# Kernel optimization log

Measured on AMD Instinct MI355X. Metric: run time of the kernel, lower is better.

## Reference

```python
import jax, jax.numpy as jnp
import numpy as np
import math

EPS_RMS = 1.1920929e-07  # torch nn.RMSNorm default eps = finfo(float32).eps
EPS_DEN = 1e-6


def rmsnorm(x, gamma):
    ms = jnp.mean(x * x, axis=-1, keepdims=True)
    return x * jax.lax.rsqrt(ms + EPS_RMS) * gamma


def setup_inputs() -> dict:
    key = jax.random.key(0)
    ks = jax.random.split(key, 8)
    B, T, K, D = 4, 4096, 256, 1024
    x_tokens = jax.random.normal(ks[0], (B, T, D), dtype=jnp.float32)
    ctx = jax.random.normal(ks[1], (B, K, D), dtype=jnp.float32)
    idx = jnp.sort(jax.random.randint(ks[2], (B, T), 0, K), axis=-1)
    s = 1.0 / math.sqrt(D)
    Wq = jax.random.normal(ks[3], (D, D), dtype=jnp.float32) * s
    Wk = jax.random.normal(ks[4], (D, D), dtype=jnp.float32) * s
    Wv = jax.random.normal(ks[5], (D, D), dtype=jnp.float32) * s
    Wo = jax.random.normal(ks[6], (D, D), dtype=jnp.float32) * s
    return {
        'x_tokens': x_tokens, 'ctx': ctx, 'ctx_index_per_token': idx,
        'gamma_q': jnp.ones((D,), jnp.float32), 'gamma_kv': jnp.ones((D,), jnp.float32),
        'Wq': Wq, 'Wk': Wk, 'Wv': Wv, 'Wo': Wo,
    }


def reference(x_tokens, ctx, ctx_index_per_token, gamma_q, gamma_kv, Wq, Wk, Wv, Wo):
    B, T, D = x_tokens.shape
    K = ctx.shape[1]
    H = 16
    hd = D // H

    def split(x):  # (B,S,D) -> (B,H,S,hd)
        return x.reshape(B, -1, H, hd).transpose(0, 2, 1, 3)

    q = split(rmsnorm(x_tokens, gamma_q) @ Wq.T)
    kn = rmsnorm(ctx, gamma_kv)
    k = split(kn @ Wk.T)
    v = split(kn @ Wv.T)

    # band mask: |ctx_pos - idx| <= 1, shape (B,1,T,K)
    ctx_pos = jnp.arange(K)[None, None, :]
    mask = (jnp.abs(ctx_pos - ctx_index_per_token[:, :, None]) <= 1)[:, None]

    scores = jnp.einsum('bhqd,bhkd->bhqk', q, k) / math.sqrt(hd)
    w = jnp.square(jax.nn.relu(scores))
    w = jnp.where(mask, w, 0.0)
    denom = jnp.maximum(w.sum(-1, keepdims=True), EPS_DEN)
    out = jnp.einsum('bhqk,bhkd->bhqd', w / denom, v)
    out = out.transpose(0, 2, 1, 3).reshape(B, T, D)
    return x_tokens + out @ Wo.T
```

## Files before the change

kernel.cpp:

```cpp
#include <hip/hip_runtime.h>
#include <hip/hip_bf16.h>
#include <stdint.h>

#define D_DIM 1024

using f32x4  = __attribute__((ext_vector_type(4))) float;
using short8 = __attribute__((ext_vector_type(8))) short;

__device__ __forceinline__ float bf2f(unsigned short u) {
    union { unsigned int i; float f; } v; v.i = ((unsigned int)u) << 16; return v.f;
}
__device__ __forceinline__ unsigned short f2bf(float f) {
    union { float f; unsigned int i; } v; v.f = f;
    unsigned int x = v.i;
    return (unsigned short)((x + 0x7fffu + ((x >> 16) & 1u)) >> 16);
}
__device__ __forceinline__ void gload16(const void* g, void* l) {
    __builtin_amdgcn_global_load_lds(
        (const __attribute__((address_space(1))) void*)g,
        (__attribute__((address_space(3))) void*)l, 16, 0, 0);
}

__global__ __launch_bounds__(256)
void convw_kernel(const float* __restrict__ Wk, const float* __restrict__ Wv,
                  const float* __restrict__ Wo, const float* __restrict__ gkv,
                  unsigned short* __restrict__ wk_hi, unsigned short* __restrict__ wk_lo,
                  unsigned short* __restrict__ wv_hi, unsigned short* __restrict__ wv_lo,
                  unsigned short* __restrict__ wo_b)
{
    const int e   = (blockIdx.x * 256 + threadIdx.x) * 4;
    const int sel = e >> 20;
    const int off = e & 0xFFFFF;
    const float* src = sel == 0 ? Wk : sel == 1 ? Wv : Wo;
    float4 v = *(const float4*)(src + off);
    if (sel < 2) {
        float4 g = *(const float4*)(gkv + (off & 1023));
        v.x *= g.x; v.y *= g.y; v.z *= g.z; v.w *= g.w;
        ushort4 h, l;
        h.x = f2bf(v.x); l.x = f2bf(v.x - bf2f(h.x));
        h.y = f2bf(v.y); l.y = f2bf(v.y - bf2f(h.y));
        h.z = f2bf(v.z); l.z = f2bf(v.z - bf2f(h.z));
        h.w = f2bf(v.w); l.w = f2bf(v.w - bf2f(h.w));
        unsigned short* hi = sel == 0 ? wk_hi : wv_hi;
        unsigned short* lo = sel == 0 ? wk_lo : wv_lo;
        *(ushort4*)(hi + off) = h;
        *(ushort4*)(lo + off) = l;
    } else {
        ushort4 o;
        o.x = f2bf(v.x); o.y = f2bf(v.y); o.z = f2bf(v.z); o.w = f2bf(v.w);
        *(ushort4*)(wo_b + off) = o;
    }
}

__global__ __launch_bounds__(256)
void transq_kernel(const float* __restrict__ Wq, const float* __restrict__ gq,
                   unsigned short* __restrict__ th, unsigned short* __restrict__ tl)
{
    __shared__ float tile[64][65];
    const int c0 = (blockIdx.x & 15) * 64;
    const int i0 = (blockIdx.x >> 4) * 64;
    const int tid = threadIdx.x;
#pragma unroll
    for (int j = 0; j < 4; ++j) {
        const int e  = tid + j * 256;
        const int rl = e >> 4;
        const int q4 = e & 15;
        float4 v = *(const float4*)(Wq + (long)(c0 + rl) * 1024 + i0 + q4 * 4);
        tile[q4 * 4 + 0][rl] = v.x;
        tile[q4 * 4 + 1][rl] = v.y;
        tile[q4 * 4 + 2][rl] = v.z;
        tile[q4 * 4 + 3][rl] = v.w;
    }
    __syncthreads();
#pragma unroll
    for (int j = 0; j < 4; ++j) {
        const int e  = tid + j * 256;
        const int il = e >> 4;
        const int s4 = e & 15;
        const float g = gq[i0 + il];
        float v0 = tile[il][s4 * 4 + 0] * g;
        float v1 = tile[il][s4 * 4 + 1] * g;
        float v2 = tile[il][s4 * 4 + 2] * g;
        float v3 = tile[il][s4 * 4 + 3] * g;
        ushort4 hh, ll;
        hh.x = f2bf(v0); ll.x = f2bf(v0 - bf2f(hh.x));
        hh.y = f2bf(v1); ll.y = f2bf(v1 - bf2f(hh.y));
        hh.z = f2bf(v2); ll.z = f2bf(v2 - bf2f(hh.z));
        hh.w = f2bf(v3); ll.w = f2bf(v3 - bf2f(hh.w));
        const long o = (long)(i0 + il) * 1024 + c0 + s4 * 4;
        *(ushort4*)(th + o) = hh;
        *(ushort4*)(tl + o) = ll;
    }
}

__global__ __launch_bounds__(256)
void rms_split_kernel(const float* __restrict__ x,
                      unsigned short* __restrict__ xh, unsigned short* __restrict__ xl)
{
    const long row = blockIdx.x;
    float4 v = ((const float4*)(x + row * D_DIM))[threadIdx.x];
    float ss = v.x*v.x + v.y*v.y + v.z*v.z + v.w*v.w;
#pragma unroll
    for (int m = 32; m; m >>= 1) ss += __shfl_xor(ss, m);
    __shared__ float red[4];
    if ((threadIdx.x & 63) == 0) red[threadIdx.x >> 6] = ss;
    __syncthreads();
    const float tot = red[0] + red[1] + red[2] + red[3];
    const float scale = rsqrtf(tot * (1.0f / 1024.0f) + 1.1920929e-07f);
    v.x *= scale; v.y *= scale; v.z *= scale; v.w *= scale;
    ushort4 h, l;
    h.x = f2bf(v.x); l.x = f2bf(v.x - bf2f(h.x));
    h.y = f2bf(v.y); l.y = f2bf(v.y - bf2f(h.y));
    h.z = f2bf(v.z); l.z = f2bf(v.z - bf2f(h.z));
    h.w = f2bf(v.w); l.w = f2bf(v.w - bf2f(h.w));
    *(ushort4*)(xh + row * D_DIM + threadIdx.x * 4) = h;
    *(ushort4*)(xl + row * D_DIM + threadIdx.x * 4) = l;
}

__global__ __launch_bounds__(256)
void gemm_kv(const unsigned short* __restrict__ ch, const unsigned short* __restrict__ cl,
             const unsigned short* __restrict__ wkh, const unsigned short* __restrict__ wkl,
             const unsigned short* __restrict__ wvh,
             unsigned short* __restrict__ kh, unsigned short* __restrict__ kl,
             float* __restrict__ v_f)
{
    __shared__ unsigned short Ah[4096], Al[4096], Bh[4096], Bl[4096];
    const bool full = (blockIdx.z == 0);
    const unsigned short* Bhp = full ? wkh : wvh;
    const unsigned short* Blp = wkl;

    const int tid = threadIdx.x, lane = tid & 63, wave = tid >> 6;
    const int wm = wave >> 1, wn = wave & 1;
    const long Arow0 = (long)blockIdx.y * 128;
    const int  Brow0 = blockIdx.x * 128;
    const int fr = lane & 15, ks = lane >> 4;
    const int ksz = (ks ^ ((fr >> 1) & 3)) << 4;
    const int kq  = ((tid & 3) ^ ((tid >> 3) & 3)) * 8;
    const int srow = tid >> 2;

    const long a_off0 = (Arow0 + srow) * D_DIM + kq;
    const long a_off1 = (Arow0 + srow + 64) * D_DIM + kq;
    const long b_off0 = (long)(Brow0 + srow) * D_DIM + kq;
    const long b_off1 = (long)(Brow0 + srow + 64) * D_DIM + kq;

    f32x4 acc[4][4] = {};
    char* AhB = (char*)Ah; char* AlB = (char*)Al;
    char* BhB = (char*)Bh; char* BlB = (char*)Bl;

    for (int kt = 0; kt < 32; ++kt) {
        const int k0 = kt * 32;
        gload16(ch + a_off0 + k0, AhB + tid * 16);
        gload16(ch + a_off1 + k0, AhB + 4096 + tid * 16);
        gload16(Bhp + b_off0 + k0, BhB + tid * 16);
        gload16(Bhp + b_off1 + k0, BhB + 4096 + tid * 16);
        if (full) {
            gload16(cl + a_off0 + k0, AlB + tid * 16);
            gload16(cl + a_off1 + k0, AlB + 4096 + tid * 16);
            gload16(Blp + b_off0 + k0, BlB + tid * 16);
            gload16(Blp + b_off1 + k0, BlB + 4096 + tid * 16);
        }
        __syncthreads();

        short8 ah[4], al[4], bh[4], bl[4];
#pragma unroll
        for (int mi = 0; mi < 4; ++mi) {
            const int aoff = (wm * 64 + mi * 16 + fr) * 64 + ksz;
            ah[mi] = *(const short8*)(AhB + aoff);
            if (full) al[mi] = *(const short8*)(AlB + aoff);
        }
#pragma unroll
        for (int ni = 0; ni < 4; ++ni) {
            const int boff = (wn * 64 + ni * 16 + fr) * 64 + ksz;
            bh[ni] = *(const short8*)(BhB + boff);
            if (full) bl[ni] = *(const short8*)(BlB + boff);
        }
#pragma unroll
        for (int mi = 0; mi < 4; ++mi)
#pragma unroll
            for (int ni = 0; ni < 4; ++ni) {
                acc[mi][ni] = __builtin_amdgcn_mfma_f32_16x16x32_bf16(ah[mi], bh[ni], acc[mi][ni], 0, 0, 0);
                if (full) {
                    acc[mi][ni] = __builtin_amdgcn_mfma_f32_16x16x32_bf16(al[mi], bh[ni], acc[mi][ni], 0, 0, 0);
                    acc[mi][ni] = __builtin_amdgcn_mfma_f32_16x16x32_bf16(ah[mi], bl[ni], acc[mi][ni], 0, 0, 0);
                }
            }
        __syncthreads();
    }

    const int c = lane & 15, r0 = (lane >> 4) * 4;
#pragma unroll
    for (int mi = 0; mi < 4; ++mi)
#pragma unroll
        for (int ni = 0; ni < 4; ++ni)
#pragma unroll
            for (int j = 0; j < 4; ++j) {
                const long row = Arow0 + wm * 64 + mi * 16 + r0 + j;
                const int  col = Brow0 + wn * 64 + ni * 16 + c;
                const float val = acc[mi][ni][j];
                if (full) {
                    const unsigned short hh = f2bf(val);
                    kh[row * D_DIM + col] = hh;
                    kl[row * D_DIM + col] = f2bf(val - bf2f(hh));
                } else {
                    v_f[row * D_DIM + col] = val;
                }
            }
}

__global__ __launch_bounds__(256)
void gemm_U(const unsigned short* __restrict__ kh, const unsigned short* __restrict__ kl,
            const unsigned short* __restrict__ th, const unsigned short* __restrict__ tl,
            unsigned short* __restrict__ Uh, unsigned short* __restrict__ Ul)
{
    __shared__ unsigned short Ah[4096], Al[4096], Bh[4096], Bl[4096];
    const int h = blockIdx.z;
    const int tid = threadIdx.x, lane = tid & 63, wave = tid >> 6;
    const int wm = wave >> 1, wn = wave & 1;
    const long Arow0 = (long)blockIdx.y * 128;
    const int  Brow0 = blockIdx.x * 128;
    const int fr = lane & 15, ks = lane >> 4;
    const int ksz = (ks ^ ((fr >> 1) & 3)) << 4;
    const int kq  = ((tid & 3) ^ ((tid >> 3) & 3)) * 8;
    const int srow = tid >> 2;
    const int kb = h * 64;

    const long a_off0 = (Arow0 + srow) * D_DIM + kb + kq;
    const long a_off1 = (Arow0 + srow + 64) * D_DIM + kb + kq;
    const long b_off0 = (long)(Brow0 + srow) * D_DIM + kb + kq;
    const long b_off1 = (long)(Brow0 + srow + 64) * D_DIM + kb + kq;

    f32x4 acc[4][4] = {};
    char* AhB = (char*)Ah; char* AlB = (char*)Al;
    char* BhB = (char*)Bh; char* BlB = (char*)Bl;

    for (int kt = 0; kt < 2; ++kt) {
        const int k0 = kt * 32;
        gload16(kh + a_off0 + k0, AhB + tid * 16);
        gload16(kh + a_off1 + k0, AhB + 4096 + tid * 16);
        gload16(kl + a_off0 + k0, AlB + tid * 16);
        gload16(kl + a_off1 + k0, AlB + 4096 + tid * 16);
        gload16(th + b_off0 + k0, BhB + tid * 16);
        gload16(th + b_off1 + k0, BhB + 4096 + tid * 16);
        gload16(tl + b_off0 + k0, BlB + tid * 16);
        gload16(tl + b_off1 + k0, BlB + 4096 + tid * 16);
        __syncthreads();

        short8 ah[4], al[4], bh[4], bl[4];
#pragma unroll
        for (int mi = 0; mi < 4; ++mi) {
            const int aoff = (wm * 64 + mi * 16 + fr) * 64 + ksz;
            ah[mi] = *(const short8*)(AhB + aoff);
            al[mi] = *(const short8*)(AlB + aoff);
        }
#pragma unroll
        for (int ni = 0; ni < 4; ++ni) {
            const int boff = (wn * 64 + ni * 16 + fr) * 64 + ksz;
            bh[ni] = *(const short8*)(BhB + boff);
            bl[ni] = *(const short8*)(BlB + boff);
        }
#pragma unroll
        for (int mi = 0; mi < 4; ++mi)
#pragma unroll
            for (int ni = 0; ni < 4; ++ni) {
                acc[mi][ni] = __builtin_amdgcn_mfma_f32_16x16x32_bf16(ah[mi], bh[ni], acc[mi][ni], 0, 0, 0);
                acc[mi][ni] = __builtin_amdgcn_mfma_f32_16x16x32_bf16(al[mi], bh[ni], acc[mi][ni], 0, 0, 0);
                acc[mi][ni] = __builtin_amdgcn_mfma_f32_16x16x32_bf16(ah[mi], bl[ni], acc[mi][ni], 0, 0, 0);
            }
        __syncthreads();
    }

    const int c = lane & 15, r0 = (lane >> 4) * 4;
#pragma unroll
    for (int mi = 0; mi < 4; ++mi)
#pragma unroll
        for (int ni = 0; ni < 4; ++ni)
#pragma unroll
            for (int j = 0; j < 4; ++j) {
                const long row = Arow0 + wm * 64 + mi * 16 + r0 + j;
                const int  col = Brow0 + wn * 64 + ni * 16 + c;
                const float val = acc[mi][ni][j];
                const long o = ((long)row * 16 + h) * 1024 + col;
                const unsigned short hh = f2bf(val);
                Uh[o] = hh;
                Ul[o] = f2bf(val - bf2f(hh));
            }
}

__global__ __launch_bounds__(256)
void score_gemm(const float* __restrict__ x, const int* __restrict__ cidx,
                const unsigned short* __restrict__ Uh, const unsigned short* __restrict__ Ul,
                float* __restrict__ sbuf, float* __restrict__ ssbuf)
{
    const int pg = blockIdx.x;
    const int mh = blockIdx.y;
    const int bz = blockIdx.z;
    const int b  = bz & 3;
    const int ksp = bz >> 2;
    const int kbase = ksp << 9;
    const int p0 = pg * 4;
    const int* ci = cidx + (b << 12);
    int l = 0, r = 4096;
    while (l < r) { int m = (l + r) >> 1; if (ci[m] < p0 - 1) l = m + 1; else r = m; }
    const int lo = l;
    r = 4096;
    while (l < r) { int m = (l + r) >> 1; if (ci[m] <= p0 + 4) l = m + 1; else r = m; }
    const int hi = l;
    if (lo + mh * 64 >= hi) return;

    float* const sb = sbuf + (long)ksp * 786432;
    float* const ssb = ssbuf + (ksp << 14);

    __shared__ unsigned short AhS[2][2048], AlS[2][2048];
    __shared__ unsigned short UhS[2][2048], UlS[2][2048];

    const int tid = threadIdx.x, lane = tid & 63, wave = tid >> 6;
    const int fr = lane & 15;
    const int ks = lane >> 4;
    const int ksz = (ks ^ ((fr >> 1) & 3)) << 4;

    const int arow = tid >> 2, aq = tid & 3;
    const int aslot = aq ^ ((arow >> 1) & 3);
    const unsigned short* const Uhb = Uh + ((long)((b << 8) + p0) * 16) * 1024 + kbase;
    const unsigned short* const Ulb = Ul + ((long)((b << 8) + p0) * 16) * 1024 + kbase;
    const float* const xb = x + ((long)b << 12) * 1024 + kbase;

    for (int t0 = lo + mh * 64; t0 < hi; t0 += 128) {
        const int tc0 = (t0 + arow < hi) ? (t0 + arow) : (hi - 1);
        const float* xr = xb + (long)tc0 * 1024 + aq * 8;
        float ss = 0.f;

        gload16(Uhb + (long)arow * 1024 + aslot * 8, (char*)&UhS[0][0] + tid * 16);
        gload16(Ulb + (long)arow * 1024 + aslot * 8, (char*)&UlS[0][0] + tid * 16);
        {
            const float4 v0 = *(const float4*)(xr);
            const float4 v1 = *(const float4*)(xr + 4);
            ss += v0.x*v0.x + v0.y*v0.y + v0.z*v0.z + v0.w*v0.w
                + v1.x*v1.x + v1.y*v1.y + v1.z*v1.z + v1.w*v1.w;
            short8 hv, lv;
            unsigned short h_;
            h_ = f2bf(v0.x); hv[0] = (short)h_; lv[0] = (short)f2bf(v0.x - bf2f(h_));
            h_ = f2bf(v0.y); hv[1] = (short)h_; lv[1] = (short)f2bf(v0.y - bf2f(h_));
            h_ = f2bf(v0.z); hv[2] = (short)h_; lv[2] = (short)f2bf(v0.z - bf2f(h_));
            h_ = f2bf(v0.w); hv[3] = (short)h_; lv[3] = (short)f2bf(v0.w - bf2f(h_));
            h_ = f2bf(v1.x); hv[4] = (short)h_; lv[4] = (short)f2bf(v1.x - bf2f(h_));
            h_ = f2bf(v1.y); hv[5] = (short)h_; lv[5] = (short)f2bf(v1.y - bf2f(h_));
            h_ = f2bf(v1.z); hv[6] = (short)h_; lv[6] = (short)f2bf(v1.z - bf2f(h_));
            h_ = f2bf(v1.w); hv[7] = (short)h_; lv[7] = (short)f2bf(v1.w - bf2f(h_));
            *(short8*)((char*)&AhS[0][0] + arow * 64 + aslot * 16) = hv;
            *(short8*)((char*)&AlS[0][0] + arow * 64 + aslot * 16) = lv;
        }
        __syncthreads();

        f32x4 acc[4] = {};
        for (int t = 0; t < 16; ++t) {
            const int cur = t & 1, nxt = cur ^ 1;
            float4 v0, v1;
            if (t < 15) {
                const int k0n = (t + 1) * 32;
                gload16(Uhb + (long)arow * 1024 + k0n + aslot * 8, (char*)&UhS[nxt][0] + tid * 16);
                gload16(Ulb + (long)arow * 1024 + k0n + aslot * 8, (char*)&UlS[nxt][0] + tid * 16);
                v0 = *(const float4*)(xr + k0n);
                v1 = *(const float4*)(xr + k0n + 4);
            }

            const int aoff = cur * 4096 + (wave * 16 + fr) * 64 + ksz;
            const short8 ah = *(const short8*)((char*)&AhS[0][0] + aoff);
            const short8 al = *(const short8*)((char*)&AlS[0][0] + aoff);
#pragma unroll
            for (int ni = 0; ni < 4; ++ni) {
                const int boff = cur * 4096 + (ni * 16 + fr) * 64 + ksz;
                const short8 uh = *(const short8*)((char*)&UhS[0][0] + boff);
                const short8 ul = *(const short8*)((char*)&UlS[0][0] + boff);
                acc[ni] = __builtin_amdgcn_mfma_f32_16x16x32_bf16(ah, uh, acc[ni], 0, 0, 0);
                acc[ni] = __builtin_amdgcn_mfma_f32_16x16x32_bf16(al, uh, acc[ni], 0, 0, 0);
                acc[ni] = __builtin_amdgcn_mfma_f32_16x16x32_bf16(ah, ul, acc[ni], 0, 0, 0);
            }

            if (t < 15) {
                ss += v0.x*v0.x + v0.y*v0.y + v0.z*v0.z + v0.w*v0.w
                    + v1.x*v1.x + v1.y*v1.y + v1.z*v1.z + v1.w*v1.w;
                short8 hv, lv;
                unsigned short h_;
                h_ = f2bf(v0.x); hv[0] = (short)h_; lv[0] = (short)f2bf(v0.x - bf2f(h_));
                h_ = f2bf(v0.y); hv[1] = (short)h_; lv[1] = (short)f2bf(v0.y - bf2f(h_));
                h_ = f2bf(v0.z); hv[2] = (short)h_; lv[2] = (short)f2bf(v0.z - bf2f(h_));
                h_ = f2bf(v0.w); hv[3] = (short)h_; lv[3] = (short)f2bf(v0.w - bf2f(h_));
                h_ = f2bf(v1.x); hv[4] = (short)h_; lv[4] = (short)f2bf(v1.x - bf2f(h_));
                h_ = f2bf(v1.y); hv[5] = (short)h_; lv[5] = (short)f2bf(v1.y - bf2f(h_));
                h_ = f2bf(v1.z); hv[6] = (short)h_; lv[6] = (short)f2bf(v1.z - bf2f(h_));
                h_ = f2bf(v1.w); hv[7] = (short)h_; lv[7] = (short)f2bf(v1.w - bf2f(h_));
                *(short8*)((char*)&AhS[0][0] + nxt * 4096 + arow * 64 + aslot * 16) = hv;
                *(short8*)((char*)&AlS[0][0] + nxt * 4096 + arow * 64 + aslot * 16) = lv;
            }
            __syncthreads();
        }

        ss += __shfl_xor(ss, 1);
        ss += __shfl_xor(ss, 2);
        if (aq == 0 && t0 + arow < hi)
            ssb[(b << 12) + t0 + arow] = ss;

        const int hcol = lane & 15;
        const int r0j = (lane >> 4) * 4;
#pragma unroll
        for (int j = 0; j < 4; ++j) {
            const int trow = t0 + wave * 16 + r0j + j;
            if (trow < hi) {
                const long tg = ((long)b << 12) + trow;
                const int idx = ci[trow];
#pragma unroll
                for (int ni = 0; ni < 4; ++ni) {
                    const int dp = p0 + ni - idx + 1;
                    if (dp >= 0 && dp <= 2)
                        sb[(tg * 16 + hcol) * 3 + dp] = acc[ni][j];
                }
            }
        }
        __syncthreads();
    }
}

__global__ __launch_bounds__(256)
void attnout_kernel(const float* __restrict__ sbuf, const float* __restrict__ ssbuf,
                    const float* __restrict__ vf, const int* __restrict__ cidx,
                    unsigned short* __restrict__ ao)
{
    const int tid = threadIdx.x;
    const int tg = tid >> 4, h = tid & 15;
    const int t = blockIdx.x * 16 + tg;
    const int b = t >> 12;
    const int idx = cidx[t];
    const float* sb0 = sbuf + ((long)t * 16 + h) * 3;
    const float* sb1 = sb0 + 786432;
    const float ssum = ssbuf[t] + ssbuf[t + 16384];
    const float scale = rsqrtf(ssum * (1.0f / 1024.0f) + 1.1920929e-07f) * 0.125f;
    float w0 = 0.f, w1 = 0.f, w2 = 0.f, wsum = 0.f;
    if (idx - 1 >= 0) { float s = (sb0[0] + sb1[0]) * scale; if (s > 0.f) { w0 = s * s; wsum += w0; } }
    { float s = (sb0[1] + sb1[1]) * scale; if (s > 0.f) { w1 = s * s; wsum += w1; } }
    if (idx + 1 < 256) { float s = (sb0[2] + sb1[2]) * scale; if (s > 0.f) { w2 = s * s; wsum += w2; } }
    const float inv = 1.0f / fmaxf(wsum, 1e-6f);
    w0 *= inv; w1 *= inv; w2 *= inv;
    const int p0 = idx > 0 ? idx - 1 : 0;
    const int p2 = idx < 255 ? idx + 1 : 255;
    const float4* v0 = (const float4*)(vf + ((long)(b * 256 + p0)) * 1024 + h * 64);
    const float4* v1 = (const float4*)(vf + ((long)(b * 256 + idx)) * 1024 + h * 64);
    const float4* v2 = (const float4*)(vf + ((long)(b * 256 + p2)) * 1024 + h * 64);
    ushort4* aop = (ushort4*)(ao + (long)t * 1024 + h * 64);
#pragma unroll
    for (int q = 0; q < 16; ++q) {
        float4 a0 = v0[q], a1 = v1[q], a2 = v2[q];
        ushort4 o;
        o.x = f2bf(w0 * a0.x + w1 * a1.x + w2 * a2.x);
        o.y = f2bf(w0 * a0.y + w1 * a1.y + w2 * a2.y);
        o.z = f2bf(w0 * a0.z + w1 * a1.z + w2 * a2.z);
        o.w = f2bf(w0 * a0.w + w1 * a1.w + w2 * a2.w);
        aop[q] = o;
    }
}

__global__ __launch_bounds__(512, 2)
void gemm_out256(const unsigned short* __restrict__ A,
                 const unsigned short* __restrict__ W,
                 float* __restrict__ C, const float* __restrict__ resid)
{
    __shared__ unsigned short As[2][8192];
    __shared__ unsigned short Bs[2][8192];

    const int lin = blockIdx.x;
    const int bx = (lin >> 3) & 3;
    const int by = ((lin >> 5) << 3) | (lin & 7);
    const long row0 = (long)by * 256;
    const int  col0 = bx * 256;

    const int tid = threadIdx.x, lane = tid & 63, wave = tid >> 6;
    const int wm = wave >> 2, wn = wave & 3;
    const int fr = lane & 15, ks = lane >> 4;
    const int ksz = (ks ^ ((fr >> 1) & 3)) << 4;
    const int kq  = ((tid & 3) ^ ((tid >> 3) & 3)) * 8;
    const int srow = tid >> 2;

    const long a_off0 = (row0 + srow) * D_DIM + kq;
    const long a_off1 = (row0 + 128 + srow) * D_DIM + kq;
    const long b_off0 = (long)(col0 + srow) * D_DIM + kq;
    const long b_off1 = (long)(col0 + 128 + srow) * D_DIM + kq;

    f32x4 acc[8][4] = {};

    gload16(A + a_off0, (char*)&As[0][0] + tid * 16);
    gload16(A + a_off1, (char*)&As[0][0] + 8192 + tid * 16);
    gload16(W + b_off0, (char*)&Bs[0][0] + tid * 16);
    gload16(W + b_off1, (char*)&Bs[0][0] + 8192 + tid * 16);

    for (int t = 0; t < 32; ++t) {
        const int cur = t & 1, nxt = cur ^ 1;
        if (t < 31) {
            const int k0 = (t + 1) * 32;
            gload16(A + a_off0 + k0, (char*)&As[nxt][0] + tid * 16);
            gload16(A + a_off1 + k0, (char*)&As[nxt][0] + 8192 + tid * 16);
            gload16(W + b_off0 + k0, (char*)&Bs[nxt][0] + tid * 16);
            gload16(W + b_off1 + k0, (char*)&Bs[nxt][0] + 8192 + tid * 16);
            asm volatile("s_waitcnt vmcnt(4)" ::: "memory");
        } else {
            asm volatile("s_waitcnt vmcnt(0)" ::: "memory");
        }
        __builtin_amdgcn_s_barrier();
        __builtin_amdgcn_sched_barrier(0);

        short8 bfrag[4];
#pragma unroll
        for (int ni = 0; ni < 4; ++ni)
            bfrag[ni] = *(const short8*)((char*)&Bs[cur][0] + (wn * 64 + ni * 16 + fr) * 64 + ksz);
        __builtin_amdgcn_s_setprio(1);
#pragma unroll
        for (int mi = 0; mi < 8; ++mi) {
            const short8 a = *(const short8*)((char*)&As[cur][0] + (wm * 128 + mi * 16 + fr) * 64 + ksz);
#pragma unroll
            for (int ni = 0; ni < 4; ++ni)
                acc[mi][ni] = __builtin_amdgcn_mfma_f32_16x16x32_bf16(a, bfrag[ni], acc[mi][ni], 0, 0, 0);
        }
        __builtin_amdgcn_s_setprio(0);
        __builtin_amdgcn_sched_barrier(0);
        __builtin_amdgcn_s_barrier();
    }

    const int c = lane & 15, rg = lane >> 4;
#pragma unroll
    for (int mi = 0; mi < 8; ++mi)
#pragma unroll
        for (int ni = 0; ni < 4; ++ni)
#pragma unroll
            for (int j = 0; j < 4; ++j) {
                const long row = row0 + wm * 128 + mi * 16 + rg * 4 + j;
                const int  col = col0 + wn * 64 + ni * 16 + c;
                C[row * D_DIM + col] = resid[row * D_DIM + col] + acc[mi][ni][j];
            }
}

extern "C" void kernel_launch(void* const* d_in, const int* in_sizes, int n_in,
                              void* d_out, int out_size, void* d_ws, size_t ws_size,
                              hipStream_t stream)
{
    const float* x    = (const float*)d_in[0];
    const float* ctx  = (const float*)d_in[1];
    const int*   cidx = (const int*)d_in[2];
    const float* gq   = (const float*)d_in[3];
    const float* gkv  = (const float*)d_in[4];
    const float* Wq   = (const float*)d_in[5];
    const float* Wk   = (const float*)d_in[6];
    const float* Wv   = (const float*)d_in[7];
    const float* Wo   = (const float*)d_in[8];
    float* out = (float*)d_out;

    char* ws = (char*)d_ws;
    const size_t MB = 1 << 20;
    unsigned short* wqT_hi = (unsigned short*)(ws + 0 * MB);
    unsigned short* wqT_lo = (unsigned short*)(ws + 2 * MB);
    unsigned short* wk_hi  = (unsigned short*)(ws + 4 * MB);
    unsigned short* wk_lo  = (unsigned short*)(ws + 6 * MB);
    unsigned short* wv_hi  = (unsigned short*)(ws + 8 * MB);
    unsigned short* wv_lo  = (unsigned short*)(ws + 10 * MB);
    unsigned short* wo_b   = (unsigned short*)(ws + 12 * MB);
    unsigned short* ch = (unsigned short*)(ws + 14 * MB);
    unsigned short* cl = (unsigned short*)(ws + 16 * MB);
    unsigned short* kh = (unsigned short*)(ws + 18 * MB);
    unsigned short* kl = (unsigned short*)(ws + 20 * MB);
    float* v_f = (float*)(ws + 22 * MB);
    unsigned short* Uh = (unsigned short*)(ws + 26 * MB);
    unsigned short* Ul = (unsigned short*)(ws + 58 * MB);
    unsigned short* ao_b = (unsigned short*)(ws + 26 * MB);
    float* sbuf  = (float*)(ws + 91 * MB);
    float* ssbuf = (float*)(ws + 97 * MB);

    convw_kernel<<<3072, 256, 0, stream>>>(Wk, Wv, Wo, gkv,
                                           wk_hi, wk_lo, wv_hi, wv_lo, wo_b);
    transq_kernel<<<256, 256, 0, stream>>>(Wq, gq, wqT_hi, wqT_lo);
    rms_split_kernel<<<1024, 256, 0, stream>>>(ctx, ch, cl);
    gemm_kv<<<dim3(8, 8, 2), 256, 0, stream>>>(ch, cl, wk_hi, wk_lo, wv_hi,
                                               kh, kl, v_f);
    gemm_U<<<dim3(8, 8, 16), 256, 0, stream>>>(kh, kl, wqT_hi, wqT_lo, Uh, Ul);
    score_gemm<<<dim3(64, 2, 8), 256, 0, stream>>>(x, cidx, Uh, Ul, sbuf, ssbuf);
    attnout_kernel<<<1024, 256, 0, stream>>>(sbuf, ssbuf, v_f, cidx, ao_b);
    gemm_out256<<<256, 512, 0, stream>>>(ao_b, wo_b, out, x);
}
```

Measured before the change: 202.8 us.

## Use four-stage LDS ring with phased loads in output GEMM

The output-projection GEMM moves from a double-buffered LDS scheme to a four-stage ring, prefetching three k-tiles ahead. Each k-step is split into two half-M phases, and the next tile's A or B loads are issued inside each phase between barriers. The aim is to hide global-to-LDS latency better and interleave loads with MFMA work. In exchange, LDS use doubles to 128KB per block, which likely drops the intended two blocks per CU to one, and the number of barriers per k-step rises.

```diff
diff --git a/kernel.cpp b/kernel.cpp
--- a/kernel.cpp
+++ b/kernel.cpp
@@ -463,8 +463,8 @@
                  const unsigned short* __restrict__ W,
                  float* __restrict__ C, const float* __restrict__ resid)
 {
-    __shared__ unsigned short As[2][8192];
-    __shared__ unsigned short Bs[2][8192];
+    __shared__ unsigned short As[4][8192];
+    __shared__ unsigned short Bs[4][8192];
 
     const int lin = blockIdx.x;
     const int bx = (lin >> 3) & 3;
@@ -486,51 +486,80 @@
 
     f32x4 acc[8][4] = {};
 
-    gload16(A + a_off0, (char*)&As[0][0] + tid * 16);
-    gload16(A + a_off1, (char*)&As[0][0] + 8192 + tid * 16);
-    gload16(W + b_off0, (char*)&Bs[0][0] + tid * 16);
-    gload16(W + b_off1, (char*)&Bs[0][0] + 8192 + tid * 16);
-
-    for (int t = 0; t < 32; ++t) {
-        const int cur = t & 1, nxt = cur ^ 1;
-        if (t < 31) {
-            const int k0 = (t + 1) * 32;
-            gload16(A + a_off0 + k0, (char*)&As[nxt][0] + tid * 16);
-            gload16(A + a_off1 + k0, (char*)&As[nxt][0] + 8192 + tid * 16);
-            gload16(W + b_off0 + k0, (char*)&Bs[nxt][0] + tid * 16);
-            gload16(W + b_off1 + k0, (char*)&Bs[nxt][0] + 8192 + tid * 16);
-            asm volatile("s_waitcnt vmcnt(4)" ::: "memory");
-        } else {
-            asm volatile("s_waitcnt vmcnt(0)" ::: "memory");
-        }
-        __builtin_amdgcn_s_barrier();
-        __builtin_amdgcn_sched_barrier(0);
-
-        short8 bfrag[4];
+#define STAGE_A(X) do { const int kofs_ = (X) * 32;                          \
+    char* base_ = (char*)&As[(X) & 3][0];                                    \
+    gload16(A + a_off0 + kofs_, base_ + tid * 16);                           \
+    gload16(A + a_off1 + kofs_, base_ + 8192 + tid * 16); } while (0)
+#define STAGE_B(X) do { const int kofs_ = (X) * 32;                          \
+    char* base_ = (char*)&Bs[(X) & 3][0];                                    \
+    gload16(W + b_off0 + kofs_, base_ + tid * 16);                           \
+    gload16(W + b_off1 + kofs_, base_ + 8192 + tid * 16); } while (0)
+
+    STAGE_A(0); STAGE_B(0); STAGE_A(1); STAGE_B(1); STAGE_A(2); STAGE_B(2);
+    asm volatile("s_waitcnt vmcnt(4)" ::: "memory");
+    __builtin_amdgcn_s_barrier();
+    __builtin_amdgcn_sched_barrier(0);
+
+    short8 bfrag[4];
+
+    for (int i = 0; i < 8; ++i) {
+        const int Tb = i * 4;
+        const bool last = (i == 7);
+#pragma unroll
+        for (int ph = 0; ph < 8; ++ph) {
+            const int tp = ph >> 1;
+            const int h  = ph & 1;
+            const int rg = tp;
+            if (h == 0) {
+#pragma unroll
+                for (int ni = 0; ni < 4; ++ni)
+                    bfrag[ni] = *(const short8*)((char*)&Bs[rg][0] +
+                                (wn * 64 + ni * 16 + fr) * 64 + ksz);
+            }
+            short8 afrag[4];
+#pragma unroll
+            for (int mi = 0; mi < 4; ++mi)
+                afrag[mi] = *(const short8*)((char*)&As[rg][0] +
+                            (wm * 128 + h * 64 + mi * 16 + fr) * 64 + ksz);
+            {
+                const int SX = Tb + 3 + tp;
+                if (SX < 32) {
+                    if (h == 0) STAGE_A(SX); else STAGE_B(SX);
+                }
+            }
+            if (ph == 3) {
+                if (last) asm volatile("s_waitcnt vmcnt(0)" ::: "memory");
+                else      asm volatile("s_waitcnt vmcnt(4)" ::: "memory");
+            } else if (ph == 7) {
+                if (!last) asm volatile("s_waitcnt vmcnt(4)" ::: "memory");
+            }
+            __builtin_amdgcn_s_barrier();
+            asm volatile("s_waitcnt lgkmcnt(0)" ::: "memory");
+            __builtin_amdgcn_sched_barrier(0);
+            __builtin_amdgcn_s_setprio(1);
+#pragma unroll
+            for (int mi = 0; mi < 4; ++mi)
+#pragma unroll
+                for (int ni = 0; ni < 4; ++ni)
+                    acc[h * 4 + mi][ni] = __builtin_amdgcn_mfma_f32_16x16x32_bf16(
+                        afrag[mi], bfrag[ni], acc[h * 4 + mi][ni], 0, 0, 0);
+            __builtin_amdgcn_s_setprio(0);
+            __builtin_amdgcn_sched_barrier(0);
+            __builtin_amdgcn_s_barrier();
+            __builtin_amdgcn_sched_barrier(0);
+        }
+    }
+#undef STAGE_A
+#undef STAGE_B
+
+    const int c = lane & 15, rg2 = lane >> 4;
+#pragma unroll
+    for (int mi = 0; mi < 8; ++mi)
 #pragma unroll
         for (int ni = 0; ni < 4; ++ni)
-            bfrag[ni] = *(const short8*)((char*)&Bs[cur][0] + (wn * 64 + ni * 16 + fr) * 64 + ksz);
-        __builtin_amdgcn_s_setprio(1);
-#pragma unroll
-        for (int mi = 0; mi < 8; ++mi) {
-            const short8 a = *(const short8*)((char*)&As[cur][0] + (wm * 128 + mi * 16 + fr) * 64 + ksz);
-#pragma unroll
-            for (int ni = 0; ni < 4; ++ni)
-                acc[mi][ni] = __builtin_amdgcn_mfma_f32_16x16x32_bf16(a, bfrag[ni], acc[mi][ni], 0, 0, 0);
-        }
-        __builtin_amdgcn_s_setprio(0);
-        __builtin_amdgcn_sched_barrier(0);
-        __builtin_amdgcn_s_barrier();
-    }
-
-    const int c = lane & 15, rg = lane >> 4;
-#pragma unroll
-    for (int mi = 0; mi < 8; ++mi)
-#pragma unroll
-        for (int ni = 0; ni < 4; ++ni)
 #pragma unroll
             for (int j = 0; j < 4; ++j) {
-                const long row = row0 + wm * 128 + mi * 16 + rg * 4 + j;
+                const long row = row0 + wm * 128 + mi * 16 + rg2 * 4 + j;
                 const int  col = col0 + wn * 64 + ni * 16 + c;
                 C[row * D_DIM + col] = resid[row * D_DIM + col] + acc[mi][ni][j];
             }
```

New measurement: 191.8 us. 1.06x faster.
